# Performance work log

Hardware: AMD Instinct MI355X
Metric: run time of the kernel (lower is better)

## Reference

```python
import jax, jax.numpy as jnp
import numpy as np

N = 50000
E = 1_600_000
IN_F = 128
OUT_F = 128
EMB = 3
KER = 4


def setup_inputs() -> dict:
    key = jax.random.key(0)
    k1, k2, k3, k4, k5 = jax.random.split(key, 5)
    x = jax.random.normal(k1, (N, IN_F), dtype=jnp.float32)
    edge_idx = jax.random.randint(k2, (2, E), 0, N, dtype=jnp.int64)
    # learned parameters (init mirrors reset_parameters, except sig=1.0 so
    # the Gaussian edge weights are non-degenerate)
    weight = 0.1 * jax.random.normal(k3, (IN_F, OUT_F, KER), dtype=jnp.float32)
    bias = 0.1 * jax.random.normal(k4, (OUT_F,), dtype=jnp.float32)
    mu = 0.005 * jax.random.normal(k5, (EMB, KER), dtype=jnp.float32)
    sig = jnp.ones((1, KER), dtype=jnp.float32)
    return {"x": x, "edge_idx": edge_idx, "weight": weight, "bias": bias, "mu": mu, "sig": sig}


def reference(x, edge_idx, weight, bias, mu, sig):
    n = x.shape[0]
    ker = weight.shape[2]
    row, col = edge_idx[0], edge_idx[1]
    domain = x[:, :3]                      # [N, 3]
    diff = domain[row] - domain[col]       # [E, 3]
    out = jnp.zeros((n, weight.shape[1]), dtype=x.dtype)
    for k in range(ker):                   # small fixed kernel loop (as in source)
        support = x @ weight[:, :, k]      # [N, out]
        # Gaussian edge weight: exp(sig_k * (-0.5 * ||diff - mu_k||^2))
        value = jnp.exp(sig[0, k] * (-0.5 * jnp.sum((diff - mu[:, k]) ** 2, axis=1)))  # [E]
        # sparse.mm(A, support): out[row] += value * support[col]
        msgs = value[:, None] * support[col]              # [E, out]
        out = out + jax.ops.segment_sum(msgs, row, num_segments=n)
    return out + bias
```

## Files before the change

### kernel.cpp

```cpp
#include <hip/hip_runtime.h>

#define IN_F 128
#define OUT_F 128
#define KER 4
#define CHUNK 16384

typedef unsigned int uint;
typedef unsigned short u16;
typedef __attribute__((ext_vector_type(8))) short bf16x8;
typedef __attribute__((ext_vector_type(4))) float f32x4;

__device__ __forceinline__ uint f2bf(float f) {
    uint u = __float_as_uint(f);
    u += 0x7fffu + ((u >> 16) & 1u);
    return u >> 16;
}


__global__ void __launch_bounds__(256) prep_kernel(
    const float* __restrict__ x, const float* __restrict__ weight,
    const float* __restrict__ mu, const float* __restrict__ sig, int n,
    u16* __restrict__ xbf, float4* __restrict__ dom, u16* __restrict__ W2p,
    float* __restrict__ kc, int nB1, int nB2) {
    const int b = blockIdx.x;
    if (b < nB1) {
        int t = b * 256 + threadIdx.x;
        if (t < n * 32) {
            float4 v = *reinterpret_cast<const float4*>(x + (size_t)t * 4);
            uint2 o;
            o.x = f2bf(v.x) | (f2bf(v.y) << 16);
            o.y = f2bf(v.z) | (f2bf(v.w) << 16);
            *reinterpret_cast<uint2*>(xbf + (size_t)t * 4) = o;
            if ((t & 31) == 0) dom[t >> 5] = make_float4(v.x, v.y, v.z, 0.f);
        }
    } else if (b < nB1 + nB2) {
        int t = (b - nB1) * 256 + threadIdx.x;
        if (t < 8192) {
            int lane = t & 63;
            int nfks = t >> 6;
            int ks = nfks & 15, nf = nfks >> 4;
            int f = nf * 16 + (lane & 15);
            int kbase = ks * 32 + ((lane >> 4) << 3);
            uint pk[4];
            #pragma unroll
            for (int jj = 0; jj < 4; ++jj) {
                int k0 = kbase + jj * 2;
                int c0 = k0 & 127, q0 = k0 >> 7;
                int k1 = k0 + 1;
                int c1 = k1 & 127, q1 = k1 >> 7;
                uint lo = f2bf(weight[((size_t)c0 * OUT_F + f) * KER + q0]);
                uint hi = f2bf(weight[((size_t)c1 * OUT_F + f) * KER + q1]);
                pk[jj] = lo | (hi << 16);
            }
            *reinterpret_cast<uint4*>(W2p + (size_t)t * 8) =
                make_uint4(pk[0], pk[1], pk[2], pk[3]);
        }
    } else {
        if (threadIdx.x < KER) {
            int k = threadIdx.x;
            float sg = sig[k];
            float m0 = mu[k], m1 = mu[KER + k], m2 = mu[2 * KER + k];
            kc[k * 5 + 0] = -0.5f * sg * (m0 * m0 + m1 * m1 + m2 * m2);
            kc[k * 5 + 1] = -0.5f * sg;
            kc[k * 5 + 2] = sg * m0;
            kc[k * 5 + 3] = sg * m1;
            kc[k * 5 + 4] = sg * m2;
        }
    }
}


__global__ void __launch_bounds__(1024) hist_kernel(
    const int* __restrict__ row, int E, int n, int nchunk,
    u16* __restrict__ hist) {
    extern __shared__ uint lds[];
    const int ch = blockIdx.x >> 2, q = blockIdx.x & 3;
    const int wq = (n + 3) >> 2;
    const int r_lo = q * wq;
    const int r_hi = min(n, r_lo + wq);
    const int width = r_hi - r_lo;
    const int words = (width + 1) >> 1;
    for (int i = threadIdx.x; i < words; i += 1024) lds[i] = 0;
    __syncthreads();
    const int base = ch * CHUNK;
    const int lim = min(base + CHUNK, E);
    for (int e = base + threadIdx.x; e < lim; e += 1024) {
        int r = row[e];
        if (r >= r_lo && r < r_hi) {
            int rr = r - r_lo;
            atomicAdd(&lds[rr >> 1], 1u << ((rr & 1) << 4));
        }
    }
    __syncthreads();
    uint* out32 = (uint*)(hist + (size_t)ch * n + r_lo);
    for (int i = threadIdx.x; i < words; i += 1024) out32[i] = lds[i];
}

__global__ void __launch_bounds__(256) colscan_kernel(
    const u16* __restrict__ hist, u16* __restrict__ bases,
    int* __restrict__ counts, int n, int nchunk) {
    int r = blockIdx.x * 256 + threadIdx.x;
    if (r >= n) return;
    uint acc = 0;
    for (int b = 0; b < nchunk; ++b) {
        uint t = hist[(size_t)b * n + r];
        bases[(size_t)b * n + r] = (u16)acc;
        acc += t;
    }
    counts[r] = (int)acc;
}

__global__ void scanA_kernel(const int* __restrict__ counts, int n, int* __restrict__ bsum) {
    __shared__ int wsum[16];
    int i = blockIdx.x * 1024 + threadIdx.x;
    int lane = threadIdx.x & 63, wv = threadIdx.x >> 6;
    int v = (i < n) ? counts[i] : 0;
    #pragma unroll
    for (int off = 32; off > 0; off >>= 1) v += __shfl_down(v, off, 64);
    if (lane == 0) wsum[wv] = v;
    __syncthreads();
    if (threadIdx.x == 0) {
        int t = 0;
        #pragma unroll
        for (int q = 0; q < 16; ++q) t += wsum[q];
        bsum[blockIdx.x] = t;
    }
}

__global__ void scanC_kernel(const int* __restrict__ counts, int n, const int* __restrict__ bsum,
                             int* __restrict__ row_ptr) {
    __shared__ int wsum[16];
    __shared__ int s_boff;
    const int tid = threadIdx.x, lane = tid & 63, wv = tid >> 6;
    const int i = blockIdx.x * 1024 + tid;
    if (tid < 64) {
        int v = (tid < blockIdx.x) ? bsum[tid] : 0;
        #pragma unroll
        for (int off = 32; off > 0; off >>= 1) v += __shfl_down(v, off, 64);
        if (tid == 0) s_boff = v;
    }
    int v = (i < n) ? counts[i] : 0;
    int s = v;
    #pragma unroll
    for (int off = 1; off < 64; off <<= 1) {
        int t = __shfl_up(s, off, 64);
        if (lane >= off) s += t;
    }
    if (lane == 63) wsum[wv] = s;
    __syncthreads();
    if (wv == 0 && lane < 16) {
        int w = wsum[lane];
        #pragma unroll
        for (int off = 1; off < 16; off <<= 1) {
            int t = __shfl_up(w, off, 64);
            if (lane >= off) w += t;
        }
        wsum[lane] = w;
    }
    __syncthreads();
    int base = s_boff + (wv ? wsum[wv - 1] : 0);
    int incl = base + s;
    if (i < n) row_ptr[i + 1] = incl;
    if (i == 0) row_ptr[0] = 0;
}

__global__ void __launch_bounds__(1024) place_kernel(
    const int* __restrict__ row, const int* __restrict__ col, int E, int n,
    const u16* __restrict__ bases, const int* __restrict__ row_ptr,
    u16* __restrict__ col_sorted) {
    extern __shared__ uint lds[];
    const int ch = blockIdx.x >> 3, x = blockIdx.x & 7;
    const int wp = (n + 7) >> 3;
    const int r_lo = x * wp;
    const int r_hi = min(n, r_lo + wp);
    const int width = r_hi - r_lo;
    const int words = (width + 1) >> 1;
    for (int i = threadIdx.x; i < words; i += 1024) lds[i] = 0;
    __syncthreads();
    const int base = ch * CHUNK;
    const int lim = min(base + CHUNK, E);
    const u16* br = bases + (size_t)ch * n;
    for (int e = base + threadIdx.x; e < lim; e += 1024) {
        int r = row[e];
        int c = col[e];
        if (r >= r_lo && r < r_hi) {
            int rr = r - r_lo;
            uint sh = (rr & 1) << 4;
            uint old = atomicAdd(&lds[rr >> 1], 1u << sh);
            int rank = (int)((old >> sh) & 0xffffu);
            int pos = row_ptr[r] + (int)br[r] + rank;
            col_sorted[pos] = (u16)c;
        }
    }
}


__global__ void __launch_bounds__(64) agg_kernel(
    const u16* __restrict__ xbf, const int* __restrict__ row_ptr,
    const u16* __restrict__ col_sorted, const float4* __restrict__ dom,
    const float* __restrict__ kc, u16* __restrict__ aggbf, int n) {
    const int i = blockIdx.x;
    const int l = threadIdx.x;
    const int start = row_ptr[i];
    const int end   = row_ptr[i + 1];
    const float4 dr = dom[i];
    float A[4], B[4], C0[4], C1[4], C2[4];
    #pragma unroll
    for (int k = 0; k < 4; ++k) {
        A[k]  = kc[k * 5 + 0];
        B[k]  = kc[k * 5 + 1];
        C0[k] = kc[k * 5 + 2];
        C1[k] = kc[k * 5 + 3];
        C2[k] = kc[k * 5 + 4];
    }

    float acc[4][2];
    #pragma unroll
    for (int k = 0; k < 4; ++k) { acc[k][0] = 0.f; acc[k][1] = 0.f; }

    auto body = [&](float qx, float qy, float qz, uint xp) {
        float d0 = dr.x - qx, d1 = dr.y - qy, d2 = dr.z - qz;
        float S = fmaf(d2, d2, fmaf(d1, d1, d0 * d0));
        float x0 = __uint_as_float(xp << 16);
        float x1 = __uint_as_float(xp & 0xffff0000u);
        #pragma unroll
        for (int k = 0; k < 4; ++k) {
            float t = fmaf(B[k], S, A[k]);
            t = fmaf(C0[k], d0, t);
            t = fmaf(C1[k], d1, t);
            t = fmaf(C2[k], d2, t);
            float v = __expf(t);
            acc[k][0] = fmaf(v, x0, acc[k][0]);
            acc[k][1] = fmaf(v, x1, acc[k][1]);
        }
    };

    int j = start;
    for (; j + 4 <= end; j += 4) {
        int c0 = col_sorted[j + 0];
        int c1 = col_sorted[j + 1];
        int c2 = col_sorted[j + 2];
        int c3 = col_sorted[j + 3];
        float4 q0 = dom[c0];
        float4 q1 = dom[c1];
        float4 q2 = dom[c2];
        float4 q3 = dom[c3];
        uint xp0 = *reinterpret_cast<const uint*>(xbf + ((size_t)c0 << 7) + (l << 1));
        uint xp1 = *reinterpret_cast<const uint*>(xbf + ((size_t)c1 << 7) + (l << 1));
        uint xp2 = *reinterpret_cast<const uint*>(xbf + ((size_t)c2 << 7) + (l << 1));
        uint xp3 = *reinterpret_cast<const uint*>(xbf + ((size_t)c3 << 7) + (l << 1));
        body(q0.x, q0.y, q0.z, xp0);
        body(q1.x, q1.y, q1.z, xp1);
        body(q2.x, q2.y, q2.z, xp2);
        body(q3.x, q3.y, q3.z, xp3);
    }
    for (; j < end; ++j) {
        int c = col_sorted[j];
        float4 q = dom[c];
        uint xp = *reinterpret_cast<const uint*>(xbf + ((size_t)c << 7) + (l << 1));
        body(q.x, q.y, q.z, xp);
    }

    u16* o = aggbf + ((size_t)i << 9) + (l << 1);
    *reinterpret_cast<uint*>(o +   0) = f2bf(acc[0][0]) | (f2bf(acc[0][1]) << 16);
    *reinterpret_cast<uint*>(o + 128) = f2bf(acc[1][0]) | (f2bf(acc[1][1]) << 16);
    *reinterpret_cast<uint*>(o + 256) = f2bf(acc[2][0]) | (f2bf(acc[2][1]) << 16);
    *reinterpret_cast<uint*>(o + 384) = f2bf(acc[3][0]) | (f2bf(acc[3][1]) << 16);
}


__global__ void __launch_bounds__(256) gemm_kernel(
    const u16* __restrict__ aggbf, const u16* __restrict__ W2p,
    const float* __restrict__ bias, float* __restrict__ out, int n) {
    const int w = threadIdx.x >> 6, l = threadIdx.x & 63;
    const int r0 = blockIdx.x * 128 + w * 32;
    int ra = r0 + (l & 15);
    int rb = ra + 16;
    if (ra > n - 1) ra = n - 1;
    if (rb > n - 1) rb = n - 1;
    const u16* pa = aggbf + ((size_t)ra << 9) + ((l >> 4) << 3);
    const u16* pb = aggbf + ((size_t)rb << 9) + ((l >> 4) << 3);
    const u16* wp = W2p + ((size_t)l << 3);

    f32x4 acc[2][8];
    #pragma unroll
    for (int m = 0; m < 2; ++m)
        #pragma unroll
        for (int nf = 0; nf < 8; ++nf)
            acc[m][nf] = (f32x4){0.f, 0.f, 0.f, 0.f};

    #pragma unroll 2
    for (int ks = 0; ks < 16; ++ks) {
        bf16x8 a0 = *reinterpret_cast<const bf16x8*>(pa + ks * 32);
        bf16x8 a1 = *reinterpret_cast<const bf16x8*>(pb + ks * 32);
        #pragma unroll
        for (int nf = 0; nf < 8; ++nf) {
            bf16x8 bfr = *reinterpret_cast<const bf16x8*>(wp + (((nf << 4) + ks) << 9));
            acc[0][nf] = __builtin_amdgcn_mfma_f32_16x16x32_bf16(a0, bfr, acc[0][nf], 0, 0, 0);
            acc[1][nf] = __builtin_amdgcn_mfma_f32_16x16x32_bf16(a1, bfr, acc[1][nf], 0, 0, 0);
        }
    }

    const int cq = l >> 4;
    const int cr = l & 15;
    #pragma unroll
    for (int nf = 0; nf < 8; ++nf) {
        float bv = bias[(nf << 4) + cr];
        #pragma unroll
        for (int m = 0; m < 2; ++m) {
            #pragma unroll
            for (int rg = 0; rg < 4; ++rg) {
                int rowi = r0 + m * 16 + cq * 4 + rg;
                if (rowi < n)
                    out[(size_t)rowi * OUT_F + (nf << 4) + cr] = acc[m][nf][rg] + bv;
            }
        }
    }
}


extern "C" void kernel_launch(void* const* d_in, const int* in_sizes, int n_in,
                              void* d_out, int out_size, void* d_ws, size_t ws_size,
                              hipStream_t stream) {
    const float* x      = (const float*)d_in[0];
    const int*   edge   = (const int*)d_in[1];
    const float* weight = (const float*)d_in[2];
    const float* bias   = (const float*)d_in[3];
    const float* mu     = (const float*)d_in[4];
    const float* sig    = (const float*)d_in[5];
    float* out = (float*)d_out;

    const int n = in_sizes[0] / IN_F;
    const int E = in_sizes[1] / 2;
    const int* row = edge;
    const int* col = edge + E;
    const int nchunk = (E + CHUNK - 1) / CHUNK;

    char* ws = (char*)d_ws;
    size_t off = 0;
    auto alloc = [&](size_t bytes) {
        size_t o = off;
        off = (off + bytes + 255) & ~(size_t)255;
        return o;
    };
    u16*    xbf        = (u16*)(ws + alloc((size_t)n * IN_F * 2));
    float4* dom        = (float4*)(ws + alloc((size_t)n * 16));
    u16*    col_sorted = (u16*)(ws + alloc((size_t)E * 2));
    u16*    aggbf      = (u16*)(ws + alloc((size_t)n * KER * IN_F * 2));
    u16*    W2p        = (u16*)(ws + alloc((size_t)KER * IN_F * OUT_F * 2));
    u16*    hist       = (u16*)(ws + alloc((size_t)nchunk * n * 2));
    u16*    bases      = (u16*)(ws + alloc((size_t)nchunk * n * 2));
    int*    counts     = (int*)(ws + alloc((size_t)n * 4));
    int*    row_ptr    = (int*)(ws + alloc(((size_t)n + 1) * 4));
    int*    bsum       = (int*)(ws + alloc(1024 * 4));
    float*  kc         = (float*)(ws + alloc(32 * 4));
    if (off > ws_size) return;

    const int nB1 = (n * 32 + 255) / 256;
    const int nB2 = 32;
    prep_kernel<<<nB1 + nB2 + 1, 256, 0, stream>>>(x, weight, mu, sig, n, xbf, dom, W2p,
                                                   kc, nB1, nB2);
    const int wq = (n + 3) >> 2;
    const size_t hist_lds = (size_t)((wq + 1) >> 1) * 4;
    hist_kernel<<<nchunk * 4, 1024, hist_lds, stream>>>(row, E, n, nchunk, hist);
    colscan_kernel<<<(n + 255) / 256, 256, 0, stream>>>(hist, bases, counts, n, nchunk);
    const int nb = (n + 1023) / 1024;
    scanA_kernel<<<nb, 1024, 0, stream>>>(counts, n, bsum);
    scanC_kernel<<<nb, 1024, 0, stream>>>(counts, n, bsum, row_ptr);
    const int wp = (n + 7) >> 3;
    const size_t place_lds = (size_t)((wp + 1) >> 1) * 4;
    place_kernel<<<nchunk * 8, 1024, place_lds, stream>>>(row, col, E, n, bases, row_ptr,
                                                          col_sorted);
    agg_kernel<<<n, 64, 0, stream>>>(xbf, row_ptr, col_sorted, dom, kc, aggbf, n);
    gemm_kernel<<<(n + 127) / 128, 256, 0, stream>>>(aggbf, W2p, bias, out, n);
}
```

Before: 316.8 us.

## Compute Gaussian edge weights once per edge in place kernel, store packed records

Moves the per-edge Gaussian weight computation out of the aggregation kernel, where all 64 lanes redundantly evaluated four exps per edge, into the scatter/place kernel, which now computes it once per edge. It writes a 16-byte record holding four bf16 weights and the column index. The aggregation kernel then only reads the record plus the bf16 feature slice, and packs four rows per 256-thread block instead of one row per 64-thread block. The cost is more memory traffic: 16-byte records instead of 2-byte column indices, written with scattered stores, and the edge weights are rounded to bf16.

```diff
diff --git a/kernel.cpp b/kernel.cpp
--- a/kernel.cpp
+++ b/kernel.cpp
@@ -167,7 +167,8 @@
 __global__ void __launch_bounds__(1024) place_kernel(
     const int* __restrict__ row, const int* __restrict__ col, int E, int n,
     const u16* __restrict__ bases, const int* __restrict__ row_ptr,
-    u16* __restrict__ col_sorted) {
+    const float4* __restrict__ dom, const float* __restrict__ kc,
+    uint4* __restrict__ recs) {
     extern __shared__ uint lds[];
     const int ch = blockIdx.x >> 3, x = blockIdx.x & 7;
     const int wp = (n + 7) >> 3;
@@ -177,33 +178,6 @@
     const int words = (width + 1) >> 1;
     for (int i = threadIdx.x; i < words; i += 1024) lds[i] = 0;
     __syncthreads();
-    const int base = ch * CHUNK;
-    const int lim = min(base + CHUNK, E);
-    const u16* br = bases + (size_t)ch * n;
-    for (int e = base + threadIdx.x; e < lim; e += 1024) {
-        int r = row[e];
-        int c = col[e];
-        if (r >= r_lo && r < r_hi) {
-            int rr = r - r_lo;
-            uint sh = (rr & 1) << 4;
-            uint old = atomicAdd(&lds[rr >> 1], 1u << sh);
-            int rank = (int)((old >> sh) & 0xffffu);
-            int pos = row_ptr[r] + (int)br[r] + rank;
-            col_sorted[pos] = (u16)c;
-        }
-    }
-}
-
-
-__global__ void __launch_bounds__(64) agg_kernel(
-    const u16* __restrict__ xbf, const int* __restrict__ row_ptr,
-    const u16* __restrict__ col_sorted, const float4* __restrict__ dom,
-    const float* __restrict__ kc, u16* __restrict__ aggbf, int n) {
-    const int i = blockIdx.x;
-    const int l = threadIdx.x;
-    const int start = row_ptr[i];
-    const int end   = row_ptr[i + 1];
-    const float4 dr = dom[i];
     float A[4], B[4], C0[4], C1[4], C2[4];
     #pragma unroll
     for (int k = 0; k < 4; ++k) {
@@ -213,52 +187,81 @@
         C1[k] = kc[k * 5 + 3];
         C2[k] = kc[k * 5 + 4];
     }
+    const int base = ch * CHUNK;
+    const int lim = min(base + CHUNK, E);
+    const u16* br = bases + (size_t)ch * n;
+    for (int e = base + threadIdx.x; e < lim; e += 1024) {
+        int r = row[e];
+        if (r >= r_lo && r < r_hi) {
+            int c = col[e];
+            float4 dr = dom[r], dc = dom[c];
+            float d0 = dr.x - dc.x, d1 = dr.y - dc.y, d2 = dr.z - dc.z;
+            float S = fmaf(d2, d2, fmaf(d1, d1, d0 * d0));
+            uint vb[4];
+            #pragma unroll
+            for (int k = 0; k < 4; ++k) {
+                float t = fmaf(B[k], S, A[k]);
+                t = fmaf(C0[k], d0, t);
+                t = fmaf(C1[k], d1, t);
+                t = fmaf(C2[k], d2, t);
+                vb[k] = f2bf(__expf(t));
+            }
+            int rr = r - r_lo;
+            uint sh = (rr & 1) << 4;
+            uint old = atomicAdd(&lds[rr >> 1], 1u << sh);
+            int rank = (int)((old >> sh) & 0xffffu);
+            int pos = row_ptr[r] + (int)br[r] + rank;
+            recs[pos] = make_uint4(vb[0] | (vb[1] << 16), vb[2] | (vb[3] << 16), (uint)c, 0u);
+        }
+    }
+}
+
+
+__global__ void __launch_bounds__(256) agg_kernel(
+    const u16* __restrict__ xbf, const int* __restrict__ row_ptr,
+    const uint4* __restrict__ recs, u16* __restrict__ aggbf, int n) {
+    const int w = threadIdx.x >> 6, l = threadIdx.x & 63;
+    const int i = blockIdx.x * 4 + w;
+    if (i >= n) return;
+    const int start = row_ptr[i];
+    const int end   = row_ptr[i + 1];
 
     float acc[4][2];
     #pragma unroll
     for (int k = 0; k < 4; ++k) { acc[k][0] = 0.f; acc[k][1] = 0.f; }
 
-    auto body = [&](float qx, float qy, float qz, uint xp) {
-        float d0 = dr.x - qx, d1 = dr.y - qy, d2 = dr.z - qz;
-        float S = fmaf(d2, d2, fmaf(d1, d1, d0 * d0));
+    auto body = [&](uint lo, uint hi, uint xp) {
         float x0 = __uint_as_float(xp << 16);
         float x1 = __uint_as_float(xp & 0xffff0000u);
-        #pragma unroll
-        for (int k = 0; k < 4; ++k) {
-            float t = fmaf(B[k], S, A[k]);
-            t = fmaf(C0[k], d0, t);
-            t = fmaf(C1[k], d1, t);
-            t = fmaf(C2[k], d2, t);
-            float v = __expf(t);
-            acc[k][0] = fmaf(v, x0, acc[k][0]);
-            acc[k][1] = fmaf(v, x1, acc[k][1]);
-        }
+        float v0 = __uint_as_float(lo << 16);
+        float v1 = __uint_as_float(lo & 0xffff0000u);
+        float v2 = __uint_as_float(hi << 16);
+        float v3 = __uint_as_float(hi & 0xffff0000u);
+        acc[0][0] = fmaf(v0, x0, acc[0][0]); acc[0][1] = fmaf(v0, x1, acc[0][1]);
+        acc[1][0] = fmaf(v1, x0, acc[1][0]); acc[1][1] = fmaf(v1, x1, acc[1][1]);
+        acc[2][0] = fmaf(v2, x0, acc[2][0]); acc[2][1] = fmaf(v2, x1, acc[2][1]);
+        acc[3][0] = fmaf(v3, x0, acc[3][0]); acc[3][1] = fmaf(v3, x1, acc[3][1]);
     };
 
     int j = start;
     for (; j + 4 <= end; j += 4) {
-        int c0 = col_sorted[j + 0];
-        int c1 = col_sorted[j + 1];
-        int c2 = col_sorted[j + 2];
-        int c3 = col_sorted[j + 3];
-        float4 q0 = dom[c0];
-        float4 q1 = dom[c1];
-        float4 q2 = dom[c2];
-        float4 q3 = dom[c3];
-        uint xp0 = *reinterpret_cast<const uint*>(xbf + ((size_t)c0 << 7) + (l << 1));
-        uint xp1 = *reinterpret_cast<const uint*>(xbf + ((size_t)c1 << 7) + (l << 1));
-        uint xp2 = *reinterpret_cast<const uint*>(xbf + ((size_t)c2 << 7) + (l << 1));
-        uint xp3 = *reinterpret_cast<const uint*>(xbf + ((size_t)c3 << 7) + (l << 1));
-        body(q0.x, q0.y, q0.z, xp0);
-        body(q1.x, q1.y, q1.z, xp1);
-        body(q2.x, q2.y, q2.z, xp2);
-        body(q3.x, q3.y, q3.z, xp3);
+        uint4 r0 = recs[j + 0];
+        uint4 r1 = recs[j + 1];
+        uint4 r2 = recs[j + 2];
+        uint4 r3 = recs[j + 3];
+        uint xp0 = *reinterpret_cast<const uint*>(xbf + ((size_t)r0.z << 7) + (l << 1));
+        uint xp1 = *reinterpret_cast<const uint*>(xbf + ((size_t)r1.z << 7) + (l << 1));
+        uint xp2 = *reinterpret_cast<const uint*>(xbf + ((size_t)r2.z << 7) + (l << 1));
+        uint xp3 = *reinterpret_cast<const uint*>(xbf + ((size_t)r3.z << 7) + (l << 1));
+        body(r0.x, r0.y, xp0);
+        body(r1.x, r1.y, xp1);
+        body(r2.x, r2.y, xp2);
+        body(r3.x, r3.y, xp3);
     }
     for (; j < end; ++j) {
-        int c = col_sorted[j];
-        float4 q = dom[c];
-        uint xp = *reinterpret_cast<const uint*>(xbf + ((size_t)c << 7) + (l << 1));
-        body(q.x, q.y, q.z, xp);
+        uint4 rc = recs[j];
+        uint xp = *reinterpret_cast<const uint*>(xbf + ((size_t)rc.z << 7) + (l << 1));
+        body(rc.x, rc.y, xp);
     }
 
     u16* o = aggbf + ((size_t)i << 9) + (l << 1);
@@ -345,7 +348,7 @@
     };
     u16*    xbf        = (u16*)(ws + alloc((size_t)n * IN_F * 2));
     float4* dom        = (float4*)(ws + alloc((size_t)n * 16));
-    u16*    col_sorted = (u16*)(ws + alloc((size_t)E * 2));
+    uint4*  recs       = (uint4*)(ws + alloc((size_t)E * 16));
     u16*    aggbf      = (u16*)(ws + alloc((size_t)n * KER * IN_F * 2));
     u16*    W2p        = (u16*)(ws + alloc((size_t)KER * IN_F * OUT_F * 2));
     u16*    hist       = (u16*)(ws + alloc((size_t)nchunk * n * 2));
@@ -370,7 +373,7 @@
     const int wp = (n + 7) >> 3;
     const size_t place_lds = (size_t)((wp + 1) >> 1) * 4;
     place_kernel<<<nchunk * 8, 1024, place_lds, stream>>>(row, col, E, n, bases, row_ptr,
-                                                          col_sorted);
-    agg_kernel<<<n, 64, 0, stream>>>(xbf, row_ptr, col_sorted, dom, kc, aggbf, n);
+                                                          dom, kc, recs);
+    agg_kernel<<<(n + 3) / 4, 256, 0, stream>>>(xbf, row_ptr, recs, aggbf, n);
     gemm_kernel<<<(n + 127) / 128, 256, 0, stream>>>(aggbf, W2p, bias, out, n);
 }
```

Result: faster. 295.6 us (-6.7%).
